# Optimization experiments

Measured on AMD Instinct MI355X. Metric: run time of the kernel, lower is better.

## Reference

```python
import jax, jax.numpy as jnp
import numpy as np

BS, N, D, H = 2, 512, 512, 16
DD = D // H
EPS = 1e-5


def _layernorm(h, g, b):
    mu = jnp.mean(h, axis=-1, keepdims=True)
    var = jnp.mean((h - mu) ** 2, axis=-1, keepdims=True)
    return (h - mu) / jnp.sqrt(var + EPS) * g + b


def setup_inputs() -> dict:
    key = jax.random.key(0)
    ks = jax.random.split(key, 10)
    x = jax.random.normal(ks[0], (BS, N, D), dtype=jnp.float32)
    u = jax.random.uniform(ks[1], (BS, N, N), dtype=jnp.float32)
    adj = jnp.where(u > 0.3, u, 0.0)
    s = 0.02
    return {
        "x": x,
        "adj": adj,
        "W_fc": jax.random.normal(ks[2], (D, D), dtype=jnp.float32) * s,
        "b_fc": jnp.zeros((D,), dtype=jnp.float32),
        "W_fc2": jax.random.normal(ks[3], (D, D), dtype=jnp.float32) * s,
        "b_fc2": jnp.zeros((D,), dtype=jnp.float32),
        "W_val": jax.random.normal(ks[4], (D, D), dtype=jnp.float32) * s,
        "b_val": jnp.zeros((D,), dtype=jnp.float32),
        "aff": jax.random.normal(ks[5], (H, DD), dtype=jnp.float32) * s,
        "aff_bias": jnp.zeros((H,), dtype=jnp.float32),
        "ln_g": jnp.ones((D,), dtype=jnp.float32),
        "ln_b": jnp.zeros((D,), dtype=jnp.float32),
        "t": 0,
    }


def reference(x, adj, W_fc, b_fc, W_fc2, b_fc2, W_val, b_val, aff, aff_bias, ln_g, ln_b, t):
    bs, n, d = x.shape
    # projections -> [bs, H, n, dd]
    def proj(W, b):
        return (x @ W.T + b).reshape(bs, n, H, DD).transpose(0, 2, 1, 3)
    x_val = proj(W_val, b_val)
    x_aff = proj(W_fc, b_fc)
    x_aff2 = proj(W_fc2, b_fc2)
    # GAT additive scores: leaky_relu over all (i,j) pairs, then dot with aff
    v = jax.nn.leaky_relu(x_aff[:, :, :, None, :] + x_aff2[:, :, None, :, :], 0.2)  # [bs,H,n,n,dd]
    scores = jnp.einsum('bhijd,hd->bhij', v, aff) + aff_bias[None, :, None, None]
    scores = jnp.where(adj[:, None, :, :] < 1e-5, jnp.float32(-1e9), scores)
    attn = jax.nn.softmax(scores, axis=-1)  # [bs,H,n,n]
    out = jnp.einsum('bhij,bhjd->bhid', attn, x_val)  # [bs,H,n,dd]
    out = out.transpose(0, 2, 1, 3).reshape(bs, n, d)
    x_aff_flat = x_aff.transpose(0, 2, 1, 3).reshape(bs, n, d)
    h = _layernorm(x_aff_flat + out, ln_g, ln_b)
    return jax.nn.relu(h)
```

## Files before the change

kernel.cpp:

```cpp
#include <hip/hip_runtime.h>


#define NB 2
#define NN 512
#define DM 512
#define NH 16
#define DD 32
#define RLOG2E 1.4426950408889634f

typedef __attribute__((ext_vector_type(8))) short bf16x8;
typedef __attribute__((ext_vector_type(4))) float f32x4;
typedef _Float16 h2 __attribute__((ext_vector_type(2)));
typedef _Float16 h8 __attribute__((ext_vector_type(8)));
typedef __fp16 fp16x2 __attribute__((ext_vector_type(2)));

__device__ __forceinline__ h2 u2h(unsigned int u) { union { unsigned int x; h2 h; } c; c.x = u; return c.h; }
__device__ __forceinline__ unsigned int h2u(h2 v) { union { unsigned int x; h2 h; } c; c.h = v; return c.x; }
__device__ __forceinline__ h8 u4h8(uint4 v) { union { uint4 u; h8 h; } c; c.u = v; return c.h; }
__device__ __forceinline__ h2 pkrtz(float x, float y) {
  union { fp16x2 a; h2 b; } c; c.a = __builtin_amdgcn_cvt_pkrtz(x, y); return c.b;
}

#if __has_builtin(__builtin_amdgcn_fdot2)
#define DOT2(a, b, c) __builtin_amdgcn_fdot2((a), (b), (c), false)
#else
#define DOT2(a, b, c) fmaf((float)(a)[0], (float)(b)[0], fmaf((float)(a)[1], (float)(b)[1], (c)))
#endif

__device__ __forceinline__ unsigned short f2bf(float f) {
  unsigned int u = __float_as_uint(f);
  u = (u + 0x7FFFu + ((u >> 16) & 1u)) >> 16;
  return (unsigned short)u;
}

__global__ void prep_kernel(const float* __restrict__ x, const float* __restrict__ w0,
                            const float* __restrict__ w1, const float* __restrict__ w2,
                            const float* __restrict__ adj,
                            unsigned short* __restrict__ xb, unsigned short* __restrict__ wb0,
                            unsigned short* __restrict__ wb1, unsigned short* __restrict__ wb2,
                            unsigned int* __restrict__ bits) {
  int gid = blockIdx.x * 256 + threadIdx.x;
  if (gid < 327680) {
    const float* src; unsigned short* dst; int off;
    if (gid < 131072)      { src = x;  dst = xb;  off = gid; }
    else if (gid < 196608) { src = w0; dst = wb0; off = gid - 131072; }
    else if (gid < 262144) { src = w1; dst = wb1; off = gid - 196608; }
    else                   { src = w2; dst = wb2; off = gid - 262144; }
    float4 v = ((const float4*)src)[off];
    ushort4 r;
    r.x = f2bf(v.x); r.y = f2bf(v.y); r.z = f2bf(v.z); r.w = f2bf(v.w);
    ((ushort4*)dst)[off] = r;
  } else {
    int t = gid - 327680;
    if (t < 16384) {
      int bb = t >> 13, rem = t & 8191;
      int i = rem >> 4, jw = rem & 15;
      const float4* ap = (const float4*)(adj + ((size_t)(bb * NN + i)) * NN + jw * 32);
      unsigned int word = 0;
      #pragma unroll
      for (int q = 0; q < 8; ++q) {
        float4 v = ap[q];
        if (v.x >= 1e-5f) word |= 1u << (q * 4 + 0);
        if (v.y >= 1e-5f) word |= 1u << (q * 4 + 1);
        if (v.z >= 1e-5f) word |= 1u << (q * 4 + 2);
        if (v.w >= 1e-5f) word |= 1u << (q * 4 + 3);
      }
      bits[((bb * 16) + jw) * 512 + i] = word;
    }
  }
}

__global__ void proj_kernel(const unsigned short* __restrict__ xb,
                            const unsigned short* __restrict__ wb0,
                            const unsigned short* __restrict__ wb1,
                            const unsigned short* __restrict__ wb2,
                            const float* __restrict__ bias0, const float* __restrict__ bias1,
                            const float* __restrict__ bias2,
                            const float* __restrict__ aff,
                            _Float16* __restrict__ Pfch, _Float16* __restrict__ Pfc2h,
                            _Float16* __restrict__ Pvalh,
                            float* __restrict__ sa, float* __restrict__ sb) {
  const int mt = blockIdx.x, nt = blockIdx.y, which = blockIdx.z;
  const unsigned short* W = (which == 0) ? wb0 : (which == 1) ? wb1 : wb2;
  const float* bias       = (which == 0) ? bias0 : (which == 1) ? bias1 : bias2;
  _Float16* Ph            = (which == 0) ? Pfch : (which == 1) ? Pfc2h : Pvalh;
  const int tid = threadIdx.x;
  const int wv = tid >> 6, lane = tid & 63;
  const int wm = wv >> 1, wn = wv & 1;
  const int mbase = mt * 64 + wm * 32, nbase = nt * 64 + wn * 32;
  const int lr = lane & 15, lk = lane >> 4;
  const bf16x8* A0 = (const bf16x8*)(xb + (size_t)(mbase + lr) * 512 + lk * 8);
  const bf16x8* A1 = (const bf16x8*)(xb + (size_t)(mbase + 16 + lr) * 512 + lk * 8);
  const bf16x8* B0 = (const bf16x8*)(W + (size_t)(nbase + lr) * 512 + lk * 8);
  const bf16x8* B1 = (const bf16x8*)(W + (size_t)(nbase + 16 + lr) * 512 + lk * 8);
  f32x4 acc00 = {0.f, 0.f, 0.f, 0.f}, acc01 = acc00, acc10 = acc00, acc11 = acc00;
  #pragma unroll
  for (int kt = 0; kt < 16; ++kt) {
    bf16x8 a0 = A0[kt * 4], a1 = A1[kt * 4];
    bf16x8 b0 = B0[kt * 4], b1 = B1[kt * 4];
    acc00 = __builtin_amdgcn_mfma_f32_16x16x32_bf16(a0, b0, acc00, 0, 0, 0);
    acc01 = __builtin_amdgcn_mfma_f32_16x16x32_bf16(a0, b1, acc01, 0, 0, 0);
    acc10 = __builtin_amdgcn_mfma_f32_16x16x32_bf16(a1, b0, acc10, 0, 0, 0);
    acc11 = __builtin_amdgcn_mfma_f32_16x16x32_bf16(a1, b1, acc11, 0, 0, 0);
  }
  const int r0 = mbase + lk * 4, cb = nbase + lr;
  const int hw = nt * 2 + wn;
  const float afA = aff[hw * 32 + lr];
  const float afB = aff[hw * 32 + lr + 16];
  float pa[4], pb[4];
  #pragma unroll
  for (int v = 0; v < 4; ++v) {
    float r00 = acc00[v] + bias[cb];
    float r01 = acc01[v] + bias[cb + 16];
    float r10 = acc10[v] + bias[cb];
    float r11 = acc11[v] + bias[cb + 16];
    Ph[(size_t)(r0 + v) * 512 + cb]           = (_Float16)r00;
    Ph[(size_t)(r0 + v) * 512 + cb + 16]      = (_Float16)r01;
    Ph[(size_t)(r0 + 16 + v) * 512 + cb]      = (_Float16)r10;
    Ph[(size_t)(r0 + 16 + v) * 512 + cb + 16] = (_Float16)r11;
    pa[v] = fmaf(afA, r00, afB * r01);
    pb[v] = fmaf(afA, r10, afB * r11);
  }
  if (which < 2) {
    #pragma unroll
    for (int m = 1; m < 16; m <<= 1) {
      #pragma unroll
      for (int v = 0; v < 4; ++v) {
        pa[v] += __shfl_xor(pa[v], m);
        pb[v] += __shfl_xor(pb[v], m);
      }
    }
    if (lr == 0) {
      float* dst = (which == 0) ? sa : sb;
      const float sc = 0.6f * RLOG2E;
      #pragma unroll
      for (int v = 0; v < 4; ++v) {
        int g0 = r0 + v, g1 = r0 + 16 + v;
        dst[((g0 >> 9) * NH + hw) * NN + (g0 & 511)] = pa[v] * sc;
        dst[((g1 >> 9) * NH + hw) * NN + (g1 & 511)] = pb[v] * sc;
      }
    }
  }
}

__launch_bounds__(256)
__global__ void attn_kernel(const _Float16* __restrict__ Pfch,
                            const _Float16* __restrict__ Pfc2h,
                            const _Float16* __restrict__ Pvalh,
                            const float* __restrict__ sa, const float* __restrict__ sb,
                            const float* __restrict__ aff,
                            const unsigned int* __restrict__ bits,
                            float* __restrict__ part_l, _Float16* __restrict__ part_oh) {
  const int bx = blockIdx.x;
  const int it = bx >> 3, jh = bx & 7;
  const int h = blockIdx.y, b = blockIdx.z;
  const int tid = threadIdx.x;
  const int w = tid >> 6, lane = tid & 63;
  const int wu = __builtin_amdgcn_readfirstlane(w);
  const int i = it * 64 + lane;
  const int jbase = jh * 64;

  __shared__ uint4 VtT4[256];
  __shared__ uint4 Pt4[512];
  __shared__ float slm[4][64];
  __shared__ float sbt[64];

  {
    const int row = tid >> 2, seg = tid & 3;
    uint4 vv = *(const uint4*)(Pvalh + ((size_t)(b * NN + jbase + row)) * DM + h * DD + seg * 8);
    _Float16* VtT_h = (_Float16*)VtT4;
    const int jc = row >> 3, jr = row & 7;
    #pragma unroll
    for (int e = 0; e < 4; ++e) {
      h2 pr = u2h(((const unsigned int*)&vv)[e]);
      int d0 = seg * 8 + 2 * e, d1 = d0 + 1;
      VtT_h[d0 * 64 + ((jc ^ (d0 & 7)) * 8) + jr] = pr[0];
      VtT_h[d1 * 64 + ((jc ^ (d1 & 7)) * 8) + jr] = pr[1];
    }
    if (tid < 64) sbt[tid] = sb[(b * NH + h) * NN + jbase + tid];
  }

  h2 ah[16], afh[16];
  {
    const uint4* ap = (const uint4*)(Pfch + ((size_t)(b * NN + i)) * DM + h * DD);
    #pragma unroll
    for (int q = 0; q < 4; ++q) {
      uint4 v0 = ap[q];
      ah[q * 4 + 0] = u2h(v0.x); ah[q * 4 + 1] = u2h(v0.y);
      ah[q * 4 + 2] = u2h(v0.z); ah[q * 4 + 3] = u2h(v0.w);
    }
    const float4* fp = (const float4*)(aff + h * DD);
    const float afs = 0.4f * RLOG2E;
    #pragma unroll
    for (int q = 0; q < 8; ++q) {
      float4 fv = fp[q];
      afh[q * 2 + 0] = pkrtz(fv.x * afs, fv.y * afs);
      afh[q * 2 + 1] = pkrtz(fv.z * afs, fv.w * afs);
    }
  }
  const float sai = sa[(b * NH + h) * NN + i];
  const unsigned int mw = bits[((b * 16) + jh * 2 + (wu >> 1)) * NN + i] >> ((wu & 1) * 16);
  float l = 0.f;
  h2 ph[8];

  const uint4* Bw = (const uint4*)(Pfc2h + ((size_t)(b * NN + jbase + wu * 16)) * DM + h * DD);

  __syncthreads();

  #pragma unroll
  for (int jp = 0; jp < 8; ++jp) {
    float pv2[2];
    #pragma unroll
    for (int q = 0; q < 2; ++q) {
      const int jo = jp * 2 + q;
      const int jl = wu * 16 + jo;
      const uint4* bp = Bw + (size_t)jo * (DM / 8);
      uint4 bq0 = bp[0], bq1 = bp[1], bq2 = bp[2], bq3 = bp[3];
      float t0 = 0.f, t1 = 0.f;
      #define SC2(k, dw, T)                                          \
        { h2 bh = u2h(dw);                                           \
          h2 u0 = u2h(h2u(ah[k] + bh) & 0x7FFF7FFFu);                \
          T = DOT2(afh[k], u0, T); }
      SC2(0,  bq0.x, t0) SC2(1,  bq0.y, t1)
      SC2(2,  bq0.z, t0) SC2(3,  bq0.w, t1)
      SC2(4,  bq1.x, t0) SC2(5,  bq1.y, t1)
      SC2(6,  bq1.z, t0) SC2(7,  bq1.w, t1)
      SC2(8,  bq2.x, t0) SC2(9,  bq2.y, t1)
      SC2(10, bq2.z, t0) SC2(11, bq2.w, t1)
      SC2(12, bq3.x, t0) SC2(13, bq3.y, t1)
      SC2(14, bq3.z, t0) SC2(15, bq3.w, t1)
      #undef SC2
      const float s = sai + sbt[jl] + (t0 + t1);
      const float p = ((mw >> jo) & 1u) ? __builtin_amdgcn_exp2f(s) : 0.f;
      l += p;
      pv2[q] = p;
    }
    ph[jp] = pkrtz(pv2[0], pv2[1]);
  }

  slm[wu][lane] = l;
  {
    const int c0 = 2 * wu, c1 = 2 * wu + 1;
    uint4 q0 = make_uint4(h2u(ph[0]), h2u(ph[1]), h2u(ph[2]), h2u(ph[3]));
    uint4 q1 = make_uint4(h2u(ph[4]), h2u(ph[5]), h2u(ph[6]), h2u(ph[7]));
    Pt4[lane * 8 + (c0 ^ (lane & 7))] = q0;
    Pt4[lane * 8 + (c1 ^ (lane & 7))] = q1;
  }
  __syncthreads();

  {
    const int lr = lane & 15, lk = lane >> 4;
    const int row = wu * 16 + lr;
    uint4 a4_0 = Pt4[row * 8 + ((lk) ^ (row & 7))];
    uint4 a4_1 = Pt4[row * 8 + ((4 + lk) ^ (row & 7))];
    #pragma unroll
    for (int ct = 0; ct < 2; ++ct) {
      const int d = ct * 16 + lr;
      uint4 b4_0 = VtT4[d * 8 + ((lk) ^ (d & 7))];
      uint4 b4_1 = VtT4[d * 8 + ((4 + lk) ^ (d & 7))];
      f32x4 acc = {0.f, 0.f, 0.f, 0.f};
      acc = __builtin_amdgcn_mfma_f32_16x16x32_f16(u4h8(a4_0), u4h8(b4_0), acc, 0, 0, 0);
      acc = __builtin_amdgcn_mfma_f32_16x16x32_f16(u4h8(a4_1), u4h8(b4_1), acc, 0, 0, 0);
      #pragma unroll
      for (int v = 0; v < 4; ++v) {
        const int grow = it * 64 + wu * 16 + lk * 4 + v;
        const size_t prow = (((size_t)(jh * 2 + b) * NH + h) * NN + grow);
        part_oh[prow * 32 + ct * 16 + lr] = (_Float16)acc[v];
      }
    }
    if (tid < 64) {
      const size_t prow = (((size_t)(jh * 2 + b) * NH + h) * NN + it * 64 + tid);
      part_l[prow] = (slm[0][tid] + slm[1][tid]) + (slm[2][tid] + slm[3][tid]);
    }
  }
}

__global__ void comb_ln_kernel(const unsigned int* __restrict__ part_o,
                               const float* __restrict__ part_l,
                               const _Float16* __restrict__ Pfch,
                               const float* __restrict__ g, const float* __restrict__ be,
                               float* __restrict__ out) {
  const int t = threadIdx.x;
  const int rg = blockIdx.x * 8 + (t >> 5);
  const int b = rg >> 9, i = rg & 511;
  const int l32 = t & 31;
  const int d0 = l32 * 16;
  const int h0 = d0 >> 5;
  const int dh = d0 & 31;
  float o[16];
  #pragma unroll
  for (int k = 0; k < 16; ++k) o[k] = 0.f;
  float L = 0.f;
  #pragma unroll
  for (int s = 0; s < 8; ++s) {
    const size_t prow = (((size_t)(s * 2 + b) * NH + h0) * NN + i);
    L += part_l[prow];
    const uint4* po = (const uint4*)(part_o + prow * 16 + (dh >> 1));
    uint4 q0 = po[0], q1 = po[1];
    #define ACC(k, dw) { h2 hh = u2h(dw); o[2*(k)] += (float)hh[0]; o[2*(k)+1] += (float)hh[1]; }
    ACC(0, q0.x) ACC(1, q0.y) ACC(2, q0.z) ACC(3, q0.w)
    ACC(4, q1.x) ACC(5, q1.y) ACC(6, q1.z) ACC(7, q1.w)
    #undef ACC
  }
  const float inv = 1.f / L;
  const uint4* pfh = (const uint4*)(Pfch + ((size_t)(b * NN + i)) * DM + d0);
  uint4 r0 = pfh[0], r1 = pfh[1];
  float pfv[16];
  #define UNP(k, dw) { h2 hh = u2h(dw); pfv[2*(k)] = (float)hh[0]; pfv[2*(k)+1] = (float)hh[1]; }
  UNP(0, r0.x) UNP(1, r0.y) UNP(2, r0.z) UNP(3, r0.w)
  UNP(4, r1.x) UNP(5, r1.y) UNP(6, r1.z) UNP(7, r1.w)
  #undef UNP
  float hv[16];
  float sS = 0.f, sQ = 0.f;
  #pragma unroll
  for (int k = 0; k < 16; ++k) {
    float hvv = pfv[k] + o[k] * inv;
    hv[k] = hvv;
    sS += hvv;
    sQ = fmaf(hvv, hvv, sQ);
  }
  #pragma unroll
  for (int off = 16; off > 0; off >>= 1) {
    sS += __shfl_xor(sS, off);
    sQ += __shfl_xor(sQ, off);
  }
  const float mu = sS * (1.f / 512.f);
  const float var = sQ * (1.f / 512.f) - mu * mu;
  const float rstd = rsqrtf(var + 1e-5f);
  float4* op = (float4*)(out + ((size_t)(b * NN + i)) * DM + d0);
  #pragma unroll
  for (int k = 0; k < 4; ++k) {
    float4 gv = ((const float4*)(g + d0))[k];
    float4 bv = ((const float4*)(be + d0))[k];
    float4 res;
    res.x = fmaxf((hv[4 * k + 0] - mu) * rstd * gv.x + bv.x, 0.f);
    res.y = fmaxf((hv[4 * k + 1] - mu) * rstd * gv.y + bv.y, 0.f);
    res.z = fmaxf((hv[4 * k + 2] - mu) * rstd * gv.z + bv.z, 0.f);
    res.w = fmaxf((hv[4 * k + 3] - mu) * rstd * gv.w + bv.w, 0.f);
    op[k] = res;
  }
}

extern "C" void kernel_launch(void* const* d_in, const int* in_sizes, int n_in,
                              void* d_out, int out_size, void* d_ws, size_t ws_size,
                              hipStream_t stream) {
  const float* x    = (const float*)d_in[0];
  const float* adj  = (const float*)d_in[1];
  const float* Wfc  = (const float*)d_in[2];
  const float* bfc  = (const float*)d_in[3];
  const float* Wfc2 = (const float*)d_in[4];
  const float* bfc2 = (const float*)d_in[5];
  const float* Wval = (const float*)d_in[6];
  const float* bval = (const float*)d_in[7];
  const float* aff  = (const float*)d_in[8];
  const float* lng  = (const float*)d_in[10];
  const float* lnb  = (const float*)d_in[11];
  float* out = (float*)d_out;

  char* ws = (char*)d_ws;
  unsigned short* xb  = (unsigned short*)(ws);
  unsigned short* wb0 = (unsigned short*)(ws + 1048576);
  unsigned short* wb1 = (unsigned short*)(ws + 1572864);
  unsigned short* wb2 = (unsigned short*)(ws + 2097152);
  _Float16* part_oh = (_Float16*)(ws);
  float* part_l   = (float*)(ws + 8388608);
  _Float16* Pfch  = (_Float16*)(ws + 8912896);
  _Float16* Pfc2h = (_Float16*)(ws + 9961472);
  _Float16* Pvalh = (_Float16*)(ws + 11010048);
  float* sa       = (float*)(ws + 12058624);
  float* sb       = (float*)(ws + 12124160);
  unsigned int* bits = (unsigned int*)(ws + 12189696);

  prep_kernel<<<1344, 256, 0, stream>>>(x, Wfc, Wfc2, Wval, adj, xb, wb0, wb1, wb2, bits);
  proj_kernel<<<dim3(16, 8, 3), 256, 0, stream>>>(xb, wb0, wb1, wb2, bfc, bfc2, bval, aff,
                                                  Pfch, Pfc2h, Pvalh, sa, sb);
  attn_kernel<<<dim3(64, 16, 2), 256, 0, stream>>>(Pfch, Pfc2h, Pvalh, sa, sb, aff, bits,
                                                   part_l, part_oh);
  comb_ln_kernel<<<128, 256, 0, stream>>>((const unsigned int*)part_oh, part_l, Pfch,
                                          lng, lnb, out);
}
```

Baseline: 56.05 us.

## Loop attention over all key chunks per block instead of split-K partials

The attention kernel now has each 512-thread block walk all eight 64-key chunks for its query tile. It accumulates P·V in MFMA registers and double-buffers the V tile in shared memory. This removes the fp16 partial-output and partial-sum writes and the combine pass, and the residual add is fused into the attention epilogue. A simpler per-row LayerNorm kernel reads an fp32 pre-norm buffer. The trade-off is far fewer blocks (256 instead of 2048), two barriers per chunk, and serialized chunk processing, which may cost parallelism.

Result: slower. 62.81 us (+12.1%).

```diff
diff --git a/kernel.cpp b/kernel.cpp
--- a/kernel.cpp
+++ b/kernel.cpp
@@ -143,42 +143,27 @@
   }
 }
 
-__launch_bounds__(256)
+__launch_bounds__(512)
 __global__ void attn_kernel(const _Float16* __restrict__ Pfch,
                             const _Float16* __restrict__ Pfc2h,
                             const _Float16* __restrict__ Pvalh,
                             const float* __restrict__ sa, const float* __restrict__ sb,
                             const float* __restrict__ aff,
                             const unsigned int* __restrict__ bits,
-                            float* __restrict__ part_l, _Float16* __restrict__ part_oh) {
-  const int bx = blockIdx.x;
-  const int it = bx >> 3, jh = bx & 7;
-  const int h = blockIdx.y, b = blockIdx.z;
+                            float* __restrict__ hpre) {
+  const int it = blockIdx.x, h = blockIdx.y, b = blockIdx.z;
   const int tid = threadIdx.x;
   const int w = tid >> 6, lane = tid & 63;
   const int wu = __builtin_amdgcn_readfirstlane(w);
   const int i = it * 64 + lane;
-  const int jbase = jh * 64;
-
-  __shared__ uint4 VtT4[256];
-  __shared__ uint4 Pt4[512];
-  __shared__ float slm[4][64];
-  __shared__ float sbt[64];
-
-  {
-    const int row = tid >> 2, seg = tid & 3;
-    uint4 vv = *(const uint4*)(Pvalh + ((size_t)(b * NN + jbase + row)) * DM + h * DD + seg * 8);
-    _Float16* VtT_h = (_Float16*)VtT4;
-    const int jc = row >> 3, jr = row & 7;
-    #pragma unroll
-    for (int e = 0; e < 4; ++e) {
-      h2 pr = u2h(((const unsigned int*)&vv)[e]);
-      int d0 = seg * 8 + 2 * e, d1 = d0 + 1;
-      VtT_h[d0 * 64 + ((jc ^ (d0 & 7)) * 8) + jr] = pr[0];
-      VtT_h[d1 * 64 + ((jc ^ (d1 & 7)) * 8) + jr] = pr[1];
-    }
-    if (tid < 64) sbt[tid] = sb[(b * NH + h) * NN + jbase + tid];
-  }
+
+  __shared__ uint4 VtT4[2][256];
+  __shared__ uint4 Pt4[2][512];
+  __shared__ float sbt[512];
+  __shared__ float slm[8][64];
+  __shared__ float srow[64];
+
+  sbt[tid] = sb[(b * NH + h) * NN + tid];
 
   h2 ah[16], afh[16];
   {
@@ -199,146 +184,138 @@
     }
   }
   const float sai = sa[(b * NH + h) * NN + i];
-  const unsigned int mw = bits[((b * 16) + jh * 2 + (wu >> 1)) * NN + i] >> ((wu & 1) * 16);
   float l = 0.f;
-  h2 ph[8];
-
-  const uint4* Bw = (const uint4*)(Pfc2h + ((size_t)(b * NN + jbase + wu * 16)) * DM + h * DD);
-
+  f32x4 acc = {0.f, 0.f, 0.f, 0.f};
+  const int lr = lane & 15, lk = lane >> 4;
+  const int rt = wu >> 1, ct = wu & 1;
+  const int srow_idx = tid >> 2, sseg = tid & 3;
+
+  uint4 vst;
+  if (tid < 256)
+    vst = *(const uint4*)(Pvalh + ((size_t)(b * NN + srow_idx)) * DM + h * DD + sseg * 8);
+  if (tid < 256) {
+    _Float16* VtT_h = (_Float16*)&VtT4[0][0];
+    const int jc = srow_idx >> 3, jr = srow_idx & 7;
+    #pragma unroll
+    for (int e = 0; e < 4; ++e) {
+      h2 pr = u2h(((const unsigned int*)&vst)[e]);
+      int d0 = sseg * 8 + 2 * e, d1 = d0 + 1;
+      VtT_h[d0 * 64 + ((jc ^ (d0 & 7)) * 8) + jr] = pr[0];
+      VtT_h[d1 * 64 + ((jc ^ (d1 & 7)) * 8) + jr] = pr[1];
+    }
+  }
   __syncthreads();
 
-  #pragma unroll
-  for (int jp = 0; jp < 8; ++jp) {
-    float pv2[2];
-    #pragma unroll
-    for (int q = 0; q < 2; ++q) {
-      const int jo = jp * 2 + q;
-      const int jl = wu * 16 + jo;
-      const uint4* bp = Bw + (size_t)jo * (DM / 8);
-      uint4 bq0 = bp[0], bq1 = bp[1], bq2 = bp[2], bq3 = bp[3];
-      float t0 = 0.f, t1 = 0.f;
-      #define SC2(k, dw, T)                                          \
-        { h2 bh = u2h(dw);                                           \
-          h2 u0 = u2h(h2u(ah[k] + bh) & 0x7FFF7FFFu);                \
-          T = DOT2(afh[k], u0, T); }
-      SC2(0,  bq0.x, t0) SC2(1,  bq0.y, t1)
-      SC2(2,  bq0.z, t0) SC2(3,  bq0.w, t1)
-      SC2(4,  bq1.x, t0) SC2(5,  bq1.y, t1)
-      SC2(6,  bq1.z, t0) SC2(7,  bq1.w, t1)
-      SC2(8,  bq2.x, t0) SC2(9,  bq2.y, t1)
-      SC2(10, bq2.z, t0) SC2(11, bq2.w, t1)
-      SC2(12, bq3.x, t0) SC2(13, bq3.y, t1)
-      SC2(14, bq3.z, t0) SC2(15, bq3.w, t1)
-      #undef SC2
-      const float s = sai + sbt[jl] + (t0 + t1);
-      const float p = ((mw >> jo) & 1u) ? __builtin_amdgcn_exp2f(s) : 0.f;
-      l += p;
-      pv2[q] = p;
-    }
-    ph[jp] = pkrtz(pv2[0], pv2[1]);
-  }
-
-  slm[wu][lane] = l;
-  {
-    const int c0 = 2 * wu, c1 = 2 * wu + 1;
-    uint4 q0 = make_uint4(h2u(ph[0]), h2u(ph[1]), h2u(ph[2]), h2u(ph[3]));
-    uint4 q1 = make_uint4(h2u(ph[4]), h2u(ph[5]), h2u(ph[6]), h2u(ph[7]));
-    Pt4[lane * 8 + (c0 ^ (lane & 7))] = q0;
-    Pt4[lane * 8 + (c1 ^ (lane & 7))] = q1;
-  }
-  __syncthreads();
-
-  {
-    const int lr = lane & 15, lk = lane >> 4;
-    const int row = wu * 16 + lr;
-    uint4 a4_0 = Pt4[row * 8 + ((lk) ^ (row & 7))];
-    uint4 a4_1 = Pt4[row * 8 + ((4 + lk) ^ (row & 7))];
-    #pragma unroll
-    for (int ct = 0; ct < 2; ++ct) {
+  for (int c = 0; c < 8; ++c) {
+    if (c < 7 && tid < 256)
+      vst = *(const uint4*)(Pvalh + ((size_t)(b * NN + (c + 1) * 64 + srow_idx)) * DM + h * DD + sseg * 8);
+
+    const uint4* Bw = (const uint4*)(Pfc2h + ((size_t)(b * NN + c * 64 + wu * 8)) * DM + h * DD);
+    const unsigned int mw =
+        bits[((b * 16) + c * 2 + (wu >> 2)) * NN + i] >> ((wu * 8) & 31);
+    h2 ph[4];
+    #pragma unroll
+    for (int jp = 0; jp < 4; ++jp) {
+      float pv2[2];
+      #pragma unroll
+      for (int q = 0; q < 2; ++q) {
+        const int jo = jp * 2 + q;
+        const uint4* bp = Bw + (size_t)jo * (DM / 8);
+        uint4 bq0 = bp[0], bq1 = bp[1], bq2 = bp[2], bq3 = bp[3];
+        float t0 = 0.f, t1 = 0.f;
+        #define SC2(k, dw, T)                                          \
+          { h2 bh = u2h(dw);                                           \
+            h2 u0 = u2h(h2u(ah[k] + bh) & 0x7FFF7FFFu);                \
+            T = DOT2(afh[k], u0, T); }
+        SC2(0,  bq0.x, t0) SC2(1,  bq0.y, t1)
+        SC2(2,  bq0.z, t0) SC2(3,  bq0.w, t1)
+        SC2(4,  bq1.x, t0) SC2(5,  bq1.y, t1)
+        SC2(6,  bq1.z, t0) SC2(7,  bq1.w, t1)
+        SC2(8,  bq2.x, t0) SC2(9,  bq2.y, t1)
+        SC2(10, bq2.z, t0) SC2(11, bq2.w, t1)
+        SC2(12, bq3.x, t0) SC2(13, bq3.y, t1)
+        SC2(14, bq3.z, t0) SC2(15, bq3.w, t1)
+        #undef SC2
+        const float s = sai + sbt[c * 64 + wu * 8 + jo] + (t0 + t1);
+        const float p = ((mw >> jo) & 1u) ? __builtin_amdgcn_exp2f(s) : 0.f;
+        l += p;
+        pv2[q] = p;
+      }
+      ph[jp] = pkrtz(pv2[0], pv2[1]);
+    }
+    Pt4[c & 1][lane * 8 + (wu ^ (lane & 7))] =
+        make_uint4(h2u(ph[0]), h2u(ph[1]), h2u(ph[2]), h2u(ph[3]));
+    __syncthreads();
+
+    {
+      const int row = rt * 16 + lr;
+      uint4 a4_0 = Pt4[c & 1][row * 8 + ((lk) ^ (row & 7))];
+      uint4 a4_1 = Pt4[c & 1][row * 8 + ((4 + lk) ^ (row & 7))];
       const int d = ct * 16 + lr;
-      uint4 b4_0 = VtT4[d * 8 + ((lk) ^ (d & 7))];
-      uint4 b4_1 = VtT4[d * 8 + ((4 + lk) ^ (d & 7))];
-      f32x4 acc = {0.f, 0.f, 0.f, 0.f};
+      uint4 b4_0 = VtT4[c & 1][d * 8 + ((lk) ^ (d & 7))];
+      uint4 b4_1 = VtT4[c & 1][d * 8 + ((4 + lk) ^ (d & 7))];
       acc = __builtin_amdgcn_mfma_f32_16x16x32_f16(u4h8(a4_0), u4h8(b4_0), acc, 0, 0, 0);
       acc = __builtin_amdgcn_mfma_f32_16x16x32_f16(u4h8(a4_1), u4h8(b4_1), acc, 0, 0, 0);
-      #pragma unroll
-      for (int v = 0; v < 4; ++v) {
-        const int grow = it * 64 + wu * 16 + lk * 4 + v;
-        const size_t prow = (((size_t)(jh * 2 + b) * NH + h) * NN + grow);
-        part_oh[prow * 32 + ct * 16 + lr] = (_Float16)acc[v];
-      }
-    }
-    if (tid < 64) {
-      const size_t prow = (((size_t)(jh * 2 + b) * NH + h) * NN + it * 64 + tid);
-      part_l[prow] = (slm[0][tid] + slm[1][tid]) + (slm[2][tid] + slm[3][tid]);
-    }
-  }
-}
-
-__global__ void comb_ln_kernel(const unsigned int* __restrict__ part_o,
-                               const float* __restrict__ part_l,
-                               const _Float16* __restrict__ Pfch,
-                               const float* __restrict__ g, const float* __restrict__ be,
-                               float* __restrict__ out) {
-  const int t = threadIdx.x;
-  const int rg = blockIdx.x * 8 + (t >> 5);
-  const int b = rg >> 9, i = rg & 511;
-  const int l32 = t & 31;
-  const int d0 = l32 * 16;
-  const int h0 = d0 >> 5;
-  const int dh = d0 & 31;
-  float o[16];
+    }
+    if (c < 7 && tid < 256) {
+      _Float16* VtT_h = (_Float16*)&VtT4[(c + 1) & 1][0];
+      const int jc = srow_idx >> 3, jr = srow_idx & 7;
+      #pragma unroll
+      for (int e = 0; e < 4; ++e) {
+        h2 pr = u2h(((const unsigned int*)&vst)[e]);
+        int d0 = sseg * 8 + 2 * e, d1 = d0 + 1;
+        VtT_h[d0 * 64 + ((jc ^ (d0 & 7)) * 8) + jr] = pr[0];
+        VtT_h[d1 * 64 + ((jc ^ (d1 & 7)) * 8) + jr] = pr[1];
+      }
+    }
+    __syncthreads();
+  }
+
+  slm[w][lane] = l;
+  __syncthreads();
+  if (w == 0) {
+    float L = 0.f;
+    #pragma unroll
+    for (int ww = 0; ww < 8; ++ww) L += slm[ww][lane];
+    srow[lane] = 1.f / L;
+  }
+  __syncthreads();
+  {
+    #pragma unroll
+    for (int v = 0; v < 4; ++v) {
+      const int row = rt * 16 + lk * 4 + v;
+      const int grow = it * 64 + row;
+      const float inv = srow[row];
+      const size_t gidx = ((size_t)(b * NN + grow)) * DM + h * DD + ct * 16 + lr;
+      const float res = (float)Pfch[gidx];
+      hpre[gidx] = fmaf(acc[v], inv, res);
+    }
+  }
+}
+
+__global__ void ln_kernel(const float* __restrict__ hpre, const float* __restrict__ g,
+                          const float* __restrict__ be, float* __restrict__ out) {
+  const int row = blockIdx.x, tid = threadIdx.x;
+  float2 v = ((const float2*)(hpre + (size_t)row * 512))[tid];
+  float s = v.x + v.y, q = v.x * v.x + v.y * v.y;
   #pragma unroll
-  for (int k = 0; k < 16; ++k) o[k] = 0.f;
-  float L = 0.f;
-  #pragma unroll
-  for (int s = 0; s < 8; ++s) {
-    const size_t prow = (((size_t)(s * 2 + b) * NH + h0) * NN + i);
-    L += part_l[prow];
-    const uint4* po = (const uint4*)(part_o + prow * 16 + (dh >> 1));
-    uint4 q0 = po[0], q1 = po[1];
-    #define ACC(k, dw) { h2 hh = u2h(dw); o[2*(k)] += (float)hh[0]; o[2*(k)+1] += (float)hh[1]; }
-    ACC(0, q0.x) ACC(1, q0.y) ACC(2, q0.z) ACC(3, q0.w)
-    ACC(4, q1.x) ACC(5, q1.y) ACC(6, q1.z) ACC(7, q1.w)
-    #undef ACC
-  }
-  const float inv = 1.f / L;
-  const uint4* pfh = (const uint4*)(Pfch + ((size_t)(b * NN + i)) * DM + d0);
-  uint4 r0 = pfh[0], r1 = pfh[1];
-  float pfv[16];
-  #define UNP(k, dw) { h2 hh = u2h(dw); pfv[2*(k)] = (float)hh[0]; pfv[2*(k)+1] = (float)hh[1]; }
-  UNP(0, r0.x) UNP(1, r0.y) UNP(2, r0.z) UNP(3, r0.w)
-  UNP(4, r1.x) UNP(5, r1.y) UNP(6, r1.z) UNP(7, r1.w)
-  #undef UNP
-  float hv[16];
-  float sS = 0.f, sQ = 0.f;
-  #pragma unroll
-  for (int k = 0; k < 16; ++k) {
-    float hvv = pfv[k] + o[k] * inv;
-    hv[k] = hvv;
-    sS += hvv;
-    sQ = fmaf(hvv, hvv, sQ);
-  }
-  #pragma unroll
-  for (int off = 16; off > 0; off >>= 1) {
-    sS += __shfl_xor(sS, off);
-    sQ += __shfl_xor(sQ, off);
-  }
-  const float mu = sS * (1.f / 512.f);
-  const float var = sQ * (1.f / 512.f) - mu * mu;
-  const float rstd = rsqrtf(var + 1e-5f);
-  float4* op = (float4*)(out + ((size_t)(b * NN + i)) * DM + d0);
-  #pragma unroll
-  for (int k = 0; k < 4; ++k) {
-    float4 gv = ((const float4*)(g + d0))[k];
-    float4 bv = ((const float4*)(be + d0))[k];
-    float4 res;
-    res.x = fmaxf((hv[4 * k + 0] - mu) * rstd * gv.x + bv.x, 0.f);
-    res.y = fmaxf((hv[4 * k + 1] - mu) * rstd * gv.y + bv.y, 0.f);
-    res.z = fmaxf((hv[4 * k + 2] - mu) * rstd * gv.z + bv.z, 0.f);
-    res.w = fmaxf((hv[4 * k + 3] - mu) * rstd * gv.w + bv.w, 0.f);
-    op[k] = res;
-  }
+  for (int off = 32; off > 0; off >>= 1) {
+    s += __shfl_xor(s, off);
+    q += __shfl_xor(q, off);
+  }
+  __shared__ float ps[4], pq[4];
+  const int w = tid >> 6, lane = tid & 63;
+  if (lane == 0) { ps[w] = s; pq[w] = q; }
+  __syncthreads();
+  s = ps[0] + ps[1] + ps[2] + ps[3];
+  q = pq[0] + pq[1] + pq[2] + pq[3];
+  float mu = s * (1.f / 512.f);
+  float var = q * (1.f / 512.f) - mu * mu;
+  float rstd = rsqrtf(var + 1e-5f);
+  float2 gv = ((const float2*)g)[tid], bv = ((const float2*)be)[tid];
+  float y0 = (v.x - mu) * rstd * gv.x + bv.x;
+  float y1 = (v.y - mu) * rstd * gv.y + bv.y;
+  ((float2*)out)[(size_t)row * 256 + tid] = make_float2(fmaxf(y0, 0.f), fmaxf(y1, 0.f));
 }
 
 extern "C" void kernel_launch(void* const* d_in, const int* in_sizes, int n_in,
@@ -362,20 +339,18 @@
   unsigned short* wb0 = (unsigned short*)(ws + 1048576);
   unsigned short* wb1 = (unsigned short*)(ws + 1572864);
   unsigned short* wb2 = (unsigned short*)(ws + 2097152);
-  _Float16* part_oh = (_Float16*)(ws);
-  float* part_l   = (float*)(ws + 8388608);
-  _Float16* Pfch  = (_Float16*)(ws + 8912896);
-  _Float16* Pfc2h = (_Float16*)(ws + 9961472);
-  _Float16* Pvalh = (_Float16*)(ws + 11010048);
-  float* sa       = (float*)(ws + 12058624);
-  float* sb       = (float*)(ws + 12124160);
-  unsigned int* bits = (unsigned int*)(ws + 12189696);
+  float* hpre     = (float*)(ws);
+  _Float16* Pfch  = (_Float16*)(ws + 2621440);
+  _Float16* Pfc2h = (_Float16*)(ws + 3670016);
+  _Float16* Pvalh = (_Float16*)(ws + 4718592);
+  float* sa       = (float*)(ws + 5767168);
+  float* sb       = (float*)(ws + 5832704);
+  unsigned int* bits = (unsigned int*)(ws + 5898240);
 
   prep_kernel<<<1344, 256, 0, stream>>>(x, Wfc, Wfc2, Wval, adj, xb, wb0, wb1, wb2, bits);
   proj_kernel<<<dim3(16, 8, 3), 256, 0, stream>>>(xb, wb0, wb1, wb2, bfc, bfc2, bval, aff,
                                                   Pfch, Pfc2h, Pvalh, sa, sb);
-  attn_kernel<<<dim3(64, 16, 2), 256, 0, stream>>>(Pfch, Pfc2h, Pvalh, sa, sb, aff, bits,
-                                                   part_l, part_oh);
-  comb_ln_kernel<<<128, 256, 0, stream>>>((const unsigned int*)part_oh, part_l, Pfch,
-                                          lng, lnb, out);
-}
+  attn_kernel<<<dim3(8, 16, 2), 512, 0, stream>>>(Pfch, Pfc2h, Pvalh, sa, sb, aff, bits,
+                                                  hpre);
+  ln_kernel<<<1024, 256, 0, stream>>>(hpre, lng, lnb, out);
+}
```

## Fuse bf16 conversion and adjacency bitmask into projection kernel; batch score loads

Applied to the files above, without the earlier changes.

Removes the separate prep kernel. The projection GEMM now loads fp32 x and weights directly and packs them to bf16 in registers with v_cvt_pk_bf16_f32. The adjacency bitmask is built by an extra z-slice of blocks in the same launch. This saves one launch and a round trip through the bf16 workspace, at the cost of the GEMM reading twice as many bytes and redoing the conversion for every tile that reuses the same data. The attention score loop also issues loads for four key rows at once before computing, to raise memory-level parallelism at the cost of more registers.

Result: slower. 62.48 us (+11.5%).

```diff
diff --git a/kernel.cpp b/kernel.cpp
--- a/kernel.cpp
+++ b/kernel.cpp
@@ -20,6 +20,14 @@
 __device__ __forceinline__ h2 pkrtz(float x, float y) {
   union { fp16x2 a; h2 b; } c; c.a = __builtin_amdgcn_cvt_pkrtz(x, y); return c.b;
 }
+__device__ __forceinline__ bf16x8 pk_bf8(float4 lo, float4 hi) {
+  union { unsigned int u[4]; bf16x8 v; } c;
+  asm("v_cvt_pk_bf16_f32 %0, %1, %2" : "=v"(c.u[0]) : "v"(lo.x), "v"(lo.y));
+  asm("v_cvt_pk_bf16_f32 %0, %1, %2" : "=v"(c.u[1]) : "v"(lo.z), "v"(lo.w));
+  asm("v_cvt_pk_bf16_f32 %0, %1, %2" : "=v"(c.u[2]) : "v"(hi.x), "v"(hi.y));
+  asm("v_cvt_pk_bf16_f32 %0, %1, %2" : "=v"(c.u[3]) : "v"(hi.z), "v"(hi.w));
+  return c.v;
+}
 
 #if __has_builtin(__builtin_amdgcn_fdot2)
 #define DOT2(a, b, c) __builtin_amdgcn_fdot2((a), (b), (c), false)
@@ -27,31 +35,20 @@
 #define DOT2(a, b, c) fmaf((float)(a)[0], (float)(b)[0], fmaf((float)(a)[1], (float)(b)[1], (c)))
 #endif
 
-__device__ __forceinline__ unsigned short f2bf(float f) {
-  unsigned int u = __float_as_uint(f);
-  u = (u + 0x7FFFu + ((u >> 16) & 1u)) >> 16;
-  return (unsigned short)u;
-}
-
-__global__ void prep_kernel(const float* __restrict__ x, const float* __restrict__ w0,
-                            const float* __restrict__ w1, const float* __restrict__ w2,
-                            const float* __restrict__ adj,
-                            unsigned short* __restrict__ xb, unsigned short* __restrict__ wb0,
-                            unsigned short* __restrict__ wb1, unsigned short* __restrict__ wb2,
+__global__ void proj_kernel(const float* __restrict__ x,
+                            const float* __restrict__ w0, const float* __restrict__ w1,
+                            const float* __restrict__ w2, const float* __restrict__ adj,
+                            const float* __restrict__ bias0, const float* __restrict__ bias1,
+                            const float* __restrict__ bias2,
+                            const float* __restrict__ aff,
+                            _Float16* __restrict__ Pfch, _Float16* __restrict__ Pfc2h,
+                            _Float16* __restrict__ Pvalh,
+                            float* __restrict__ sa, float* __restrict__ sb,
                             unsigned int* __restrict__ bits) {
-  int gid = blockIdx.x * 256 + threadIdx.x;
-  if (gid < 327680) {
-    const float* src; unsigned short* dst; int off;
-    if (gid < 131072)      { src = x;  dst = xb;  off = gid; }
-    else if (gid < 196608) { src = w0; dst = wb0; off = gid - 131072; }
-    else if (gid < 262144) { src = w1; dst = wb1; off = gid - 196608; }
-    else                   { src = w2; dst = wb2; off = gid - 262144; }
-    float4 v = ((const float4*)src)[off];
-    ushort4 r;
-    r.x = f2bf(v.x); r.y = f2bf(v.y); r.z = f2bf(v.z); r.w = f2bf(v.w);
-    ((ushort4*)dst)[off] = r;
-  } else {
-    int t = gid - 327680;
+  const int which = blockIdx.z;
+  const int tid = threadIdx.x;
+  if (which == 3) {
+    int t = (blockIdx.x * 8 + blockIdx.y) * 256 + tid;
     if (t < 16384) {
       int bb = t >> 13, rem = t & 8191;
       int i = rem >> 4, jw = rem & 15;
@@ -67,37 +64,27 @@
       }
       bits[((bb * 16) + jw) * 512 + i] = word;
     }
-  }
-}
-
-__global__ void proj_kernel(const unsigned short* __restrict__ xb,
-                            const unsigned short* __restrict__ wb0,
-                            const unsigned short* __restrict__ wb1,
-                            const unsigned short* __restrict__ wb2,
-                            const float* __restrict__ bias0, const float* __restrict__ bias1,
-                            const float* __restrict__ bias2,
-                            const float* __restrict__ aff,
-                            _Float16* __restrict__ Pfch, _Float16* __restrict__ Pfc2h,
-                            _Float16* __restrict__ Pvalh,
-                            float* __restrict__ sa, float* __restrict__ sb) {
-  const int mt = blockIdx.x, nt = blockIdx.y, which = blockIdx.z;
-  const unsigned short* W = (which == 0) ? wb0 : (which == 1) ? wb1 : wb2;
-  const float* bias       = (which == 0) ? bias0 : (which == 1) ? bias1 : bias2;
-  _Float16* Ph            = (which == 0) ? Pfch : (which == 1) ? Pfc2h : Pvalh;
-  const int tid = threadIdx.x;
+    return;
+  }
+  const float* W     = (which == 0) ? w0 : (which == 1) ? w1 : w2;
+  const float* bias  = (which == 0) ? bias0 : (which == 1) ? bias1 : bias2;
+  _Float16* Ph       = (which == 0) ? Pfch : (which == 1) ? Pfc2h : Pvalh;
+  const int mt = blockIdx.x, nt = blockIdx.y;
   const int wv = tid >> 6, lane = tid & 63;
   const int wm = wv >> 1, wn = wv & 1;
   const int mbase = mt * 64 + wm * 32, nbase = nt * 64 + wn * 32;
   const int lr = lane & 15, lk = lane >> 4;
-  const bf16x8* A0 = (const bf16x8*)(xb + (size_t)(mbase + lr) * 512 + lk * 8);
-  const bf16x8* A1 = (const bf16x8*)(xb + (size_t)(mbase + 16 + lr) * 512 + lk * 8);
-  const bf16x8* B0 = (const bf16x8*)(W + (size_t)(nbase + lr) * 512 + lk * 8);
-  const bf16x8* B1 = (const bf16x8*)(W + (size_t)(nbase + 16 + lr) * 512 + lk * 8);
+  const float4* A0f = (const float4*)(x + (size_t)(mbase + lr) * 512 + lk * 8);
+  const float4* A1f = (const float4*)(x + (size_t)(mbase + 16 + lr) * 512 + lk * 8);
+  const float4* B0f = (const float4*)(W + (size_t)(nbase + lr) * 512 + lk * 8);
+  const float4* B1f = (const float4*)(W + (size_t)(nbase + 16 + lr) * 512 + lk * 8);
   f32x4 acc00 = {0.f, 0.f, 0.f, 0.f}, acc01 = acc00, acc10 = acc00, acc11 = acc00;
   #pragma unroll
   for (int kt = 0; kt < 16; ++kt) {
-    bf16x8 a0 = A0[kt * 4], a1 = A1[kt * 4];
-    bf16x8 b0 = B0[kt * 4], b1 = B1[kt * 4];
+    bf16x8 a0 = pk_bf8(A0f[kt * 8], A0f[kt * 8 + 1]);
+    bf16x8 a1 = pk_bf8(A1f[kt * 8], A1f[kt * 8 + 1]);
+    bf16x8 b0 = pk_bf8(B0f[kt * 8], B0f[kt * 8 + 1]);
+    bf16x8 b1 = pk_bf8(B1f[kt * 8], B1f[kt * 8 + 1]);
     acc00 = __builtin_amdgcn_mfma_f32_16x16x32_bf16(a0, b0, acc00, 0, 0, 0);
     acc01 = __builtin_amdgcn_mfma_f32_16x16x32_bf16(a0, b1, acc01, 0, 0, 0);
     acc10 = __builtin_amdgcn_mfma_f32_16x16x32_bf16(a1, b0, acc10, 0, 0, 0);
@@ -208,34 +195,37 @@
   __syncthreads();
 
   #pragma unroll
-  for (int jp = 0; jp < 8; ++jp) {
-    float pv2[2];
-    #pragma unroll
-    for (int q = 0; q < 2; ++q) {
-      const int jo = jp * 2 + q;
-      const int jl = wu * 16 + jo;
-      const uint4* bp = Bw + (size_t)jo * (DM / 8);
-      uint4 bq0 = bp[0], bq1 = bp[1], bq2 = bp[2], bq3 = bp[3];
+  for (int g = 0; g < 4; ++g) {
+    uint4 bq[4][4];
+    #pragma unroll
+    for (int jj = 0; jj < 4; ++jj) {
+      const uint4* bp = Bw + (size_t)(g * 4 + jj) * (DM / 8);
+      bq[jj][0] = bp[0]; bq[jj][1] = bp[1]; bq[jj][2] = bp[2]; bq[jj][3] = bp[3];
+    }
+    float pg[4];
+    #pragma unroll
+    for (int jj = 0; jj < 4; ++jj) {
+      const int jo = g * 4 + jj;
       float t0 = 0.f, t1 = 0.f;
       #define SC2(k, dw, T)                                          \
         { h2 bh = u2h(dw);                                           \
           h2 u0 = u2h(h2u(ah[k] + bh) & 0x7FFF7FFFu);                \
           T = DOT2(afh[k], u0, T); }
-      SC2(0,  bq0.x, t0) SC2(1,  bq0.y, t1)
-      SC2(2,  bq0.z, t0) SC2(3,  bq0.w, t1)
-      SC2(4,  bq1.x, t0) SC2(5,  bq1.y, t1)
-      SC2(6,  bq1.z, t0) SC2(7,  bq1.w, t1)
-      SC2(8,  bq2.x, t0) SC2(9,  bq2.y, t1)
-      SC2(10, bq2.z, t0) SC2(11, bq2.w, t1)
-      SC2(12, bq3.x, t0) SC2(13, bq3.y, t1)
-      SC2(14, bq3.z, t0) SC2(15, bq3.w, t1)
+      SC2(0,  bq[jj][0].x, t0) SC2(1,  bq[jj][0].y, t1)
+      SC2(2,  bq[jj][0].z, t0) SC2(3,  bq[jj][0].w, t1)
+      SC2(4,  bq[jj][1].x, t0) SC2(5,  bq[jj][1].y, t1)
+      SC2(6,  bq[jj][1].z, t0) SC2(7,  bq[jj][1].w, t1)
+      SC2(8,  bq[jj][2].x, t0) SC2(9,  bq[jj][2].y, t1)
+      SC2(10, bq[jj][2].z, t0) SC2(11, bq[jj][2].w, t1)
+      SC2(12, bq[jj][3].x, t0) SC2(13, bq[jj][3].y, t1)
+      SC2(14, bq[jj][3].z, t0) SC2(15, bq[jj][3].w, t1)
       #undef SC2
-      const float s = sai + sbt[jl] + (t0 + t1);
-      const float p = ((mw >> jo) & 1u) ? __builtin_amdgcn_exp2f(s) : 0.f;
-      l += p;
-      pv2[q] = p;
-    }
-    ph[jp] = pkrtz(pv2[0], pv2[1]);
+      const float s = sai + sbt[wu * 16 + jo] + (t0 + t1);
+      pg[jj] = ((mw >> jo) & 1u) ? __builtin_amdgcn_exp2f(s) : 0.f;
+      l += pg[jj];
+    }
+    ph[g * 2]     = pkrtz(pg[0], pg[1]);
+    ph[g * 2 + 1] = pkrtz(pg[2], pg[3]);
   }
 
   slm[wu][lane] = l;
@@ -358,10 +348,6 @@
   float* out = (float*)d_out;
 
   char* ws = (char*)d_ws;
-  unsigned short* xb  = (unsigned short*)(ws);
-  unsigned short* wb0 = (unsigned short*)(ws + 1048576);
-  unsigned short* wb1 = (unsigned short*)(ws + 1572864);
-  unsigned short* wb2 = (unsigned short*)(ws + 2097152);
   _Float16* part_oh = (_Float16*)(ws);
   float* part_l   = (float*)(ws + 8388608);
   _Float16* Pfch  = (_Float16*)(ws + 8912896);
@@ -371,9 +357,8 @@
   float* sb       = (float*)(ws + 12124160);
   unsigned int* bits = (unsigned int*)(ws + 12189696);
 
-  prep_kernel<<<1344, 256, 0, stream>>>(x, Wfc, Wfc2, Wval, adj, xb, wb0, wb1, wb2, bits);
-  proj_kernel<<<dim3(16, 8, 3), 256, 0, stream>>>(xb, wb0, wb1, wb2, bfc, bfc2, bval, aff,
-                                                  Pfch, Pfc2h, Pvalh, sa, sb);
+  proj_kernel<<<dim3(16, 8, 4), 256, 0, stream>>>(x, Wfc, Wfc2, Wval, adj, bfc, bfc2, bval,
+                                                  aff, Pfch, Pfc2h, Pvalh, sa, sb, bits);
   attn_kernel<<<dim3(64, 16, 2), 256, 0, stream>>>(Pfch, Pfc2h, Pvalh, sa, sb, aff, bits,
                                                    part_l, part_oh);
   comb_ln_kernel<<<128, 256, 0, stream>>>((const unsigned int*)part_oh, part_l, Pfch,
```

## Run attention tile with a single wavefront per block, removing block syncs

Applied to the files above, without the earlier changes.

Each attention block now has one 64-lane wavefront instead of four. That wavefront processes all 64 key columns of its tile serially and does all four MFMA row tiles itself. This drops the __syncthreads barriers and the cross-wave shared-memory reduction of the softmax denominator. The cost is four times less parallelism per block (2048 small blocks), more serial work per wave and a longer dependency chain. Occupancy then depends on how many small blocks fit per CU.

Result: slower. 61.14 us (+9.1%).

```diff
diff --git a/kernel.cpp b/kernel.cpp
--- a/kernel.cpp
+++ b/kernel.cpp
@@ -143,7 +143,7 @@
   }
 }
 
-__launch_bounds__(256)
+__launch_bounds__(64)
 __global__ void attn_kernel(const _Float16* __restrict__ Pfch,
                             const _Float16* __restrict__ Pfc2h,
                             const _Float16* __restrict__ Pvalh,
@@ -154,30 +154,31 @@
   const int bx = blockIdx.x;
   const int it = bx >> 3, jh = bx & 7;
   const int h = blockIdx.y, b = blockIdx.z;
-  const int tid = threadIdx.x;
-  const int w = tid >> 6, lane = tid & 63;
-  const int wu = __builtin_amdgcn_readfirstlane(w);
+  const int lane = threadIdx.x;
   const int i = it * 64 + lane;
   const int jbase = jh * 64;
 
   __shared__ uint4 VtT4[256];
   __shared__ uint4 Pt4[512];
-  __shared__ float slm[4][64];
   __shared__ float sbt[64];
 
+  sbt[lane] = sb[(b * NH + h) * NN + jbase + lane];
   {
-    const int row = tid >> 2, seg = tid & 3;
-    uint4 vv = *(const uint4*)(Pvalh + ((size_t)(b * NN + jbase + row)) * DM + h * DD + seg * 8);
     _Float16* VtT_h = (_Float16*)VtT4;
-    const int jc = row >> 3, jr = row & 7;
-    #pragma unroll
-    for (int e = 0; e < 4; ++e) {
-      h2 pr = u2h(((const unsigned int*)&vv)[e]);
-      int d0 = seg * 8 + 2 * e, d1 = d0 + 1;
-      VtT_h[d0 * 64 + ((jc ^ (d0 & 7)) * 8) + jr] = pr[0];
-      VtT_h[d1 * 64 + ((jc ^ (d1 & 7)) * 8) + jr] = pr[1];
-    }
-    if (tid < 64) sbt[tid] = sb[(b * NH + h) * NN + jbase + tid];
+    #pragma unroll
+    for (int q = 0; q < 4; ++q) {
+      const int cidx = q * 64 + lane;
+      const int row = cidx >> 2, seg = cidx & 3;
+      uint4 vv = *(const uint4*)(Pvalh + ((size_t)(b * NN + jbase + row)) * DM + h * DD + seg * 8);
+      const int jc = row >> 3, jr = row & 7;
+      #pragma unroll
+      for (int e = 0; e < 4; ++e) {
+        h2 pr = u2h(((const unsigned int*)&vv)[e]);
+        int d0 = seg * 8 + 2 * e, d1 = d0 + 1;
+        VtT_h[d0 * 64 + ((jc ^ (d0 & 7)) * 8) + jr] = pr[0];
+        VtT_h[d1 * 64 + ((jc ^ (d1 & 7)) * 8) + jr] = pr[1];
+      }
+    }
   }
 
   h2 ah[16], afh[16];
@@ -199,78 +200,77 @@
     }
   }
   const float sai = sa[(b * NH + h) * NN + i];
-  const unsigned int mw = bits[((b * 16) + jh * 2 + (wu >> 1)) * NN + i] >> ((wu & 1) * 16);
+  const unsigned int mw0 = bits[((b * 16) + jh * 2) * NN + i];
+  const unsigned int mw1 = bits[((b * 16) + jh * 2 + 1) * NN + i];
   float l = 0.f;
-  h2 ph[8];
-
-  const uint4* Bw = (const uint4*)(Pfc2h + ((size_t)(b * NN + jbase + wu * 16)) * DM + h * DD);
-
-  __syncthreads();
-
-  #pragma unroll
-  for (int jp = 0; jp < 8; ++jp) {
-    float pv2[2];
-    #pragma unroll
-    for (int q = 0; q < 2; ++q) {
-      const int jo = jp * 2 + q;
-      const int jl = wu * 16 + jo;
-      const uint4* bp = Bw + (size_t)jo * (DM / 8);
-      uint4 bq0 = bp[0], bq1 = bp[1], bq2 = bp[2], bq3 = bp[3];
-      float t0 = 0.f, t1 = 0.f;
-      #define SC2(k, dw, T)                                          \
-        { h2 bh = u2h(dw);                                           \
-          h2 u0 = u2h(h2u(ah[k] + bh) & 0x7FFF7FFFu);                \
-          T = DOT2(afh[k], u0, T); }
-      SC2(0,  bq0.x, t0) SC2(1,  bq0.y, t1)
-      SC2(2,  bq0.z, t0) SC2(3,  bq0.w, t1)
-      SC2(4,  bq1.x, t0) SC2(5,  bq1.y, t1)
-      SC2(6,  bq1.z, t0) SC2(7,  bq1.w, t1)
-      SC2(8,  bq2.x, t0) SC2(9,  bq2.y, t1)
-      SC2(10, bq2.z, t0) SC2(11, bq2.w, t1)
-      SC2(12, bq3.x, t0) SC2(13, bq3.y, t1)
-      SC2(14, bq3.z, t0) SC2(15, bq3.w, t1)
-      #undef SC2
-      const float s = sai + sbt[jl] + (t0 + t1);
-      const float p = ((mw >> jo) & 1u) ? __builtin_amdgcn_exp2f(s) : 0.f;
-      l += p;
-      pv2[q] = p;
-    }
-    ph[jp] = pkrtz(pv2[0], pv2[1]);
-  }
-
-  slm[wu][lane] = l;
-  {
-    const int c0 = 2 * wu, c1 = 2 * wu + 1;
-    uint4 q0 = make_uint4(h2u(ph[0]), h2u(ph[1]), h2u(ph[2]), h2u(ph[3]));
-    uint4 q1 = make_uint4(h2u(ph[4]), h2u(ph[5]), h2u(ph[6]), h2u(ph[7]));
-    Pt4[lane * 8 + (c0 ^ (lane & 7))] = q0;
-    Pt4[lane * 8 + (c1 ^ (lane & 7))] = q1;
-  }
-  __syncthreads();
+
+  const uint4* Bw = (const uint4*)(Pfc2h + ((size_t)(b * NN + jbase)) * DM + h * DD);
+
+  #pragma unroll 2
+  for (int c = 0; c < 8; ++c) {
+    const unsigned int mwc = (c < 4) ? mw0 : mw1;
+    h2 ph[4];
+    #pragma unroll
+    for (int jp = 0; jp < 4; ++jp) {
+      float pv2[2];
+      #pragma unroll
+      for (int q = 0; q < 2; ++q) {
+        const int jo = c * 8 + jp * 2 + q;
+        const uint4* bp = Bw + (size_t)jo * (DM / 8);
+        uint4 bq0 = bp[0], bq1 = bp[1], bq2 = bp[2], bq3 = bp[3];
+        float t0 = 0.f, t1 = 0.f;
+        #define SC2(k, dw, T)                                          \
+          { h2 bh = u2h(dw);                                           \
+            h2 u0 = u2h(h2u(ah[k] + bh) & 0x7FFF7FFFu);                \
+            T = DOT2(afh[k], u0, T); }
+        SC2(0,  bq0.x, t0) SC2(1,  bq0.y, t1)
+        SC2(2,  bq0.z, t0) SC2(3,  bq0.w, t1)
+        SC2(4,  bq1.x, t0) SC2(5,  bq1.y, t1)
+        SC2(6,  bq1.z, t0) SC2(7,  bq1.w, t1)
+        SC2(8,  bq2.x, t0) SC2(9,  bq2.y, t1)
+        SC2(10, bq2.z, t0) SC2(11, bq2.w, t1)
+        SC2(12, bq3.x, t0) SC2(13, bq3.y, t1)
+        SC2(14, bq3.z, t0) SC2(15, bq3.w, t1)
+        #undef SC2
+        const float s = sai + sbt[jo] + (t0 + t1);
+        const float p = ((mwc >> (jo & 31)) & 1u) ? __builtin_amdgcn_exp2f(s) : 0.f;
+        l += p;
+        pv2[q] = p;
+      }
+      ph[jp] = pkrtz(pv2[0], pv2[1]);
+    }
+    Pt4[lane * 8 + (c ^ (lane & 7))] =
+        make_uint4(h2u(ph[0]), h2u(ph[1]), h2u(ph[2]), h2u(ph[3]));
+  }
+
+  part_l[(((size_t)(jh * 2 + b) * NH + h) * NN + i)] = l;
 
   {
     const int lr = lane & 15, lk = lane >> 4;
-    const int row = wu * 16 + lr;
-    uint4 a4_0 = Pt4[row * 8 + ((lk) ^ (row & 7))];
-    uint4 a4_1 = Pt4[row * 8 + ((4 + lk) ^ (row & 7))];
+    uint4 b4[2][2];
     #pragma unroll
     for (int ct = 0; ct < 2; ++ct) {
       const int d = ct * 16 + lr;
-      uint4 b4_0 = VtT4[d * 8 + ((lk) ^ (d & 7))];
-      uint4 b4_1 = VtT4[d * 8 + ((4 + lk) ^ (d & 7))];
-      f32x4 acc = {0.f, 0.f, 0.f, 0.f};
-      acc = __builtin_amdgcn_mfma_f32_16x16x32_f16(u4h8(a4_0), u4h8(b4_0), acc, 0, 0, 0);
-      acc = __builtin_amdgcn_mfma_f32_16x16x32_f16(u4h8(a4_1), u4h8(b4_1), acc, 0, 0, 0);
-      #pragma unroll
-      for (int v = 0; v < 4; ++v) {
-        const int grow = it * 64 + wu * 16 + lk * 4 + v;
-        const size_t prow = (((size_t)(jh * 2 + b) * NH + h) * NN + grow);
-        part_oh[prow * 32 + ct * 16 + lr] = (_Float16)acc[v];
-      }
-    }
-    if (tid < 64) {
-      const size_t prow = (((size_t)(jh * 2 + b) * NH + h) * NN + it * 64 + tid);
-      part_l[prow] = (slm[0][tid] + slm[1][tid]) + (slm[2][tid] + slm[3][tid]);
+      b4[ct][0] = VtT4[d * 8 + ((lk) ^ (d & 7))];
+      b4[ct][1] = VtT4[d * 8 + ((4 + lk) ^ (d & 7))];
+    }
+    #pragma unroll
+    for (int rt = 0; rt < 4; ++rt) {
+      const int row = rt * 16 + lr;
+      uint4 a4_0 = Pt4[row * 8 + ((lk) ^ (row & 7))];
+      uint4 a4_1 = Pt4[row * 8 + ((4 + lk) ^ (row & 7))];
+      #pragma unroll
+      for (int ct = 0; ct < 2; ++ct) {
+        f32x4 acc = {0.f, 0.f, 0.f, 0.f};
+        acc = __builtin_amdgcn_mfma_f32_16x16x32_f16(u4h8(a4_0), u4h8(b4[ct][0]), acc, 0, 0, 0);
+        acc = __builtin_amdgcn_mfma_f32_16x16x32_f16(u4h8(a4_1), u4h8(b4[ct][1]), acc, 0, 0, 0);
+        #pragma unroll
+        for (int v = 0; v < 4; ++v) {
+          const int grow = it * 64 + rt * 16 + lk * 4 + v;
+          const size_t prow = (((size_t)(jh * 2 + b) * NH + h) * NN + grow);
+          part_oh[prow * 32 + ct * 16 + lr] = (_Float16)acc[v];
+        }
+      }
     }
   }
 }
@@ -374,8 +374,8 @@
   prep_kernel<<<1344, 256, 0, stream>>>(x, Wfc, Wfc2, Wval, adj, xb, wb0, wb1, wb2, bits);
   proj_kernel<<<dim3(16, 8, 3), 256, 0, stream>>>(xb, wb0, wb1, wb2, bfc, bfc2, bval, aff,
                                                   Pfch, Pfc2h, Pvalh, sa, sb);
-  attn_kernel<<<dim3(64, 16, 2), 256, 0, stream>>>(Pfch, Pfc2h, Pvalh, sa, sb, aff, bits,
-                                                   part_l, part_oh);
+  attn_kernel<<<dim3(64, 16, 2), 64, 0, stream>>>(Pfch, Pfc2h, Pvalh, sa, sb, aff, bits,
+                                                  part_l, part_oh);
   comb_ln_kernel<<<128, 256, 0, stream>>>((const unsigned int*)part_oh, part_l, Pfch,
                                           lng, lnb, out);
 }
```
